# Optimization experiments

Measured on AMD Instinct MI355X. Metric: run time of the kernel, lower is better.

## Reference

```python
import jax, jax.numpy as jnp
import numpy as np

DIM = 1024
N_HEADS = 16
HEAD_DIM = DIM // N_HEADS
COND_DIM = 1024
MLP_RATIO = 4
B, S = 4, 1024
LN_EPS = 1e-5


def _layer_norm(x, w):
    # F.layer_norm without affine bias, then * weight (per original LayerNorm)
    x32 = x.astype(jnp.float32)
    mu = jnp.mean(x32, axis=-1, keepdims=True)
    var = jnp.var(x32, axis=-1, keepdims=True)
    return (x32 - mu) * jax.lax.rsqrt(var + LN_EPS) * w


def _rope(t, cos, sin):
    # t: [b, s, h, d]; cos/sin: [s, d/2]; rotate-half convention
    d2 = t.shape[-1] // 2
    t1, t2 = t[..., :d2], t[..., d2:]
    c = cos[None, :, None, :]
    s = sin[None, :, None, :]
    return jnp.concatenate([t1 * c - t2 * s, t2 * c + t1 * s], axis=-1)


def setup_inputs() -> dict:
    key = jax.random.key(0)
    ks = jax.random.split(key, 12)
    inv_freq = 1.0 / (10000.0 ** (np.arange(0, HEAD_DIM, 2) / HEAD_DIM))
    ang = np.arange(S)[:, None] * inv_freq[None, :]
    return {
        "x": jax.random.normal(ks[0], (B, S, DIM), jnp.float32),
        "cos": jnp.asarray(np.cos(ang), jnp.float32),
        "sin": jnp.asarray(np.sin(ang), jnp.float32),
        "c": jax.random.normal(ks[1], (B, COND_DIM), jnp.float32),
        "w_ln1": jnp.ones((DIM,), jnp.float32),
        "w_ln2": jnp.ones((DIM,), jnp.float32),
        "w_qkv": jax.random.normal(ks[2], (DIM, 3 * DIM), jnp.float32) * 0.02,
        "w_attn_out": jax.random.normal(ks[3], (DIM, DIM), jnp.float32) * 0.02,
        "w_mlp1": jax.random.normal(ks[4], (DIM, MLP_RATIO * DIM), jnp.float32) * 0.02,
        "b_mlp1": jnp.zeros((MLP_RATIO * DIM,), jnp.float32),
        "w_mlp2": jax.random.normal(ks[5], (MLP_RATIO * DIM, DIM), jnp.float32) * 0.02,
        "b_mlp2": jnp.zeros((DIM,), jnp.float32),
        "w_ada": jax.random.normal(ks[6], (COND_DIM, 6 * DIM), jnp.float32) * 0.02,
        "b_ada": jax.random.normal(ks[7], (6 * DIM,), jnp.float32) * 0.02,
    }


def reference(x, cos, sin, c, w_ln1, w_ln2, w_qkv, w_attn_out,
              w_mlp1, b_mlp1, w_mlp2, b_mlp2, w_ada, b_ada):
    b, s, dim = x.shape
    # adaLN modulation: [b, 6*dim] -> six [b, 1, dim] chunks
    mod = (c @ w_ada + b_ada)[:, None, :]
    shift_msa, scale_msa, gate_msa, shift_mlp, scale_mlp, gate_mlp = jnp.split(mod, 6, axis=2)

    x_skip = x
    h = _layer_norm(x, w_ln1) * (1.0 + scale_msa) + shift_msa
    qkv = (h @ w_qkv).reshape(b, s, 3, N_HEADS, HEAD_DIM)
    q = _rope(qkv[:, :, 0], cos, sin)
    k = _rope(qkv[:, :, 1], cos, sin)
    v = qkv[:, :, 2]

    scale = 1.0 / jnp.sqrt(jnp.asarray(HEAD_DIM, x.dtype))
    scores = jnp.einsum('bshd,bthd->bhst', q, k) * scale  # [b,h,s,s]
    attn = jax.nn.softmax(scores, axis=-1)
    o = jnp.einsum('bhst,bthd->bshd', attn, v).reshape(b, s, dim)

    x = x_skip + gate_msa * (o @ w_attn_out)

    h2 = _layer_norm(x, w_ln2) * (1.0 + scale_mlp) + shift_mlp
    m = jax.nn.gelu(h2 @ w_mlp1 + b_mlp1, approximate=True) @ w_mlp2 + b_mlp2
    return x + gate_mlp * m
```

## Files before the change

kernel.cpp:

```cpp
#include <hip/hip_runtime.h>
#include <stdint.h>

typedef unsigned short u16;
typedef __bf16 bf16x8 __attribute__((ext_vector_type(8)));
typedef float f32x4 __attribute__((ext_vector_type(4)));

#define MOD6  6144

__device__ __forceinline__ float b2f(unsigned int u) {
    union { unsigned int i; float f; } z; z.i = u << 16; return z.f;
}
__device__ __forceinline__ u16 f2b(float f) {
    union { float f; unsigned int i; } z; z.f = f;
    unsigned int i = z.i;
    return (u16)((i + 0x7fffu + ((i >> 16) & 1u)) >> 16);
}
union U4 { uint4 u; u16 s[8]; };
union U2 { uint2 u; u16 s[4]; };
union B8 { bf16x8 v; unsigned int w[4]; };

__device__ __forceinline__ float ldf(const void* p, size_t i, int isbf) {
    if (isbf) return b2f(((const u16*)p)[i]);
    return ((const float*)p)[i];
}
__device__ __forceinline__ void load4(const void* p, size_t i, int isbf, float* v) {
    if (isbf) {
        U2 t; t.u = *(const uint2*)((const u16*)p + i);
#pragma unroll
        for (int e = 0; e < 4; e++) v[e] = b2f(t.s[e]);
    } else {
        float4 f = *(const float4*)((const float*)p + i);
        v[0] = f.x; v[1] = f.y; v[2] = f.z; v[3] = f.w;
    }
}

__device__ __forceinline__ void gld16(u16* lds, const u16* g) {
    __builtin_amdgcn_global_load_lds(
        (__attribute__((address_space(1))) void*)(g),
        (__attribute__((address_space(3))) void*)(lds), 16, 0, 0);
}

__global__ void detect_dtype(const unsigned int* __restrict__ w, int* __restrict__ flag) {
    if (threadIdx.x == 0 && blockIdx.x == 0)
        *flag = (w[0] == 0x3F803F80u) ? 1 : 0;
}

__global__ void transpose_any(const void* __restrict__ in, u16* __restrict__ out,
                              int K, int N, const int* __restrict__ flag) {
    const int isbf = *flag;
    __shared__ u16 tile[64][66];
    const int ntn = N >> 6;
    const int k0 = (blockIdx.x / ntn) << 6;
    const int n0 = (blockIdx.x % ntn) << 6;
    const int tid = threadIdx.x;
    const int r = tid >> 3;
    const int c = (tid & 7) * 8;
#pragma unroll
    for (int rr = 0; rr < 64; rr += 32) {
        const size_t base = (size_t)(k0 + r + rr) * N + n0 + c;
        u16* t = &tile[r + rr][c];
        if (isbf) {
            U4 v; v.u = *(const uint4*)((const u16*)in + base);
#pragma unroll
            for (int e = 0; e < 8; e++) t[e] = v.s[e];
        } else {
            float4 a = *(const float4*)((const float*)in + base);
            float4 b = *(const float4*)((const float*)in + base + 4);
            t[0] = f2b(a.x); t[1] = f2b(a.y); t[2] = f2b(a.z); t[3] = f2b(a.w);
            t[4] = f2b(b.x); t[5] = f2b(b.y); t[6] = f2b(b.z); t[7] = f2b(b.w);
        }
    }
    __syncthreads();
#pragma unroll
    for (int rr = 0; rr < 64; rr += 32) {
        U4 v;
#pragma unroll
        for (int e = 0; e < 8; e++) v.s[e] = tile[c + e][r + rr];
        *(uint4*)&out[(size_t)(n0 + r + rr) * K + k0 + c] = v.u;
    }
}

__global__ void ada_partial(const void* __restrict__ c, const void* __restrict__ w_ada,
                            float* __restrict__ part, const int* __restrict__ flag) {
    const int isbf = *flag;
    const int g = blockIdx.x * 256 + threadIdx.x;
    const int slice = g / 24576;
    const int idx = g - slice * 24576;
    const int b = idx / MOD6, n = idx - (idx / MOD6) * MOD6;
    const int k0 = slice * 128;
    float acc = 0.f;
    if (isbf) {
        const u16* cr = (const u16*)c + b * 1024 + k0;
        const u16* wp = (const u16*)w_ada + (size_t)k0 * MOD6 + n;
#pragma unroll 8
        for (int k = 0; k < 128; k++)
            acc += b2f(cr[k]) * b2f(wp[(size_t)k * MOD6]);
    } else {
        const float* cr = (const float*)c + b * 1024 + k0;
        const float* wp = (const float*)w_ada + (size_t)k0 * MOD6 + n;
#pragma unroll 8
        for (int k = 0; k < 128; k++)
            acc += cr[k] * wp[(size_t)k * MOD6];
    }
    part[g] = acc;
}
__global__ void ada_reduce(const float* __restrict__ part, const void* __restrict__ b_ada,
                           float* __restrict__ mod, const int* __restrict__ flag) {
    const int g = blockIdx.x * 256 + threadIdx.x;
    float acc = ldf(b_ada, g % MOD6, *flag);
#pragma unroll
    for (int s = 0; s < 8; s++) acc += part[s * 24576 + g];
    mod[g] = acc;
}

__global__ void ln_mod_kernel(const void* __restrict__ x, const void* __restrict__ w,
                              const float* __restrict__ mod, int shift_off,
                              int scale_off, u16* __restrict__ out,
                              const int* __restrict__ flag, int x_is_f32) {
    const int isbf = *flag;
    const int xb = x_is_f32 ? 0 : isbf;
    const int tk = blockIdx.x;
    const int b = tk >> 10;
    const int tid = threadIdx.x;
    float v[4];
    load4(x, (size_t)tk * 1024 + tid * 4, xb, v);
    float s = v[0] + v[1] + v[2] + v[3];
    float ss = v[0]*v[0] + v[1]*v[1] + v[2]*v[2] + v[3]*v[3];
#pragma unroll
    for (int off = 1; off < 64; off <<= 1) {
        s  += __shfl_xor(s, off);
        ss += __shfl_xor(ss, off);
    }
    __shared__ float ls[4], lss[4];
    if ((tid & 63) == 0) { ls[tid >> 6] = s; lss[tid >> 6] = ss; }
    __syncthreads();
    s  = ls[0] + ls[1] + ls[2] + ls[3];
    ss = lss[0] + lss[1] + lss[2] + lss[3];
    const float mu  = s * (1.f / 1024.f);
    const float var = ss * (1.f / 1024.f) - mu * mu;
    const float rstd = rsqrtf(var + 1e-5f);
    float wv[4];
    load4(w, (size_t)tid * 4, isbf, wv);
    const float* mb = mod + (size_t)b * MOD6;
    U2 o;
#pragma unroll
    for (int e = 0; e < 4; e++) {
        const int col = tid * 4 + e;
        float n = (v[e] - mu) * rstd * wv[e];
        o.s[e] = f2b(n * (1.f + mb[scale_off + col]) + mb[shift_off + col]);
    }
    *(uint2*)(out + (size_t)tk * 1024 + tid * 4) = o.u;
}

__global__ void out_init(const float* __restrict__ res, const float* __restrict__ gate,
                         const void* __restrict__ bias, float* __restrict__ out,
                         const int* __restrict__ flag) {
    const int isbf = *flag;
    const int g = blockIdx.x * 256 + threadIdx.x;
    const int col = (g & 255) * 4;
    const int row = g >> 8;
    const int b = row >> 10;
    float bv[4];
    load4(bias, (size_t)col, isbf, bv);
    const float* gp = gate + (size_t)b * MOD6 + col;
    float4 r = *(const float4*)(res + (size_t)row * 1024 + col);
    float4 o;
    o.x = r.x + gp[0] * bv[0];
    o.y = r.y + gp[1] * bv[1];
    o.z = r.z + gp[2] * bv[2];
    o.w = r.w + gp[3] * bv[3];
    *(float4*)(out + (size_t)row * 1024 + col) = o;
}

#define EPI_STORE 0
#define EPI_RES_GATE 1
#define EPI_GELU_BIAS 2
#define EPI_RES_GATE_BIAS 3
#define EPI_ATOMIC_GATE 4

template <int EPI>
__launch_bounds__(256, 2)
__global__ void gemm_bt(const u16* __restrict__ A, const u16* __restrict__ Bt,
                        void* __restrict__ Cv, int M, int N, int K,
                        const void* __restrict__ res, const float* __restrict__ gate,
                        const void* __restrict__ bias, const int* __restrict__ flag,
                        int Ks) {
    __shared__ __align__(16) u16 sA[128 * 32];
    __shared__ __align__(16) u16 sB[128 * 32];
    const int isbf = flag ? *flag : 0;
    const int tid = threadIdx.x;
    const int lane = tid & 63;
    const int w = tid >> 6;
    const int wm = w >> 1, wn = w & 1;
    const int c16 = lane & 15, quad = lane >> 4;
    const int m0 = blockIdx.y * 128, n0 = blockIdx.x * 128;
    const int kt0 = blockIdx.z * Ks;

    const int srow = lane >> 2;
    const int schunk = lane & 3;
    const int gchunk = schunk ^ (srow & 3);

    const u16* gA = A + (size_t)m0 * K + 8 * gchunk;
    const u16* gB = Bt + (size_t)n0 * K + 8 * gchunk;
    const int cs = quad ^ (c16 & 3);

    f32x4 acc[4][4];
#pragma unroll
    for (int i = 0; i < 4; i++)
#pragma unroll
        for (int j = 0; j < 4; j++) acc[i][j] = (f32x4){0.f, 0.f, 0.f, 0.f};

#pragma unroll 1
    for (int kt = kt0; kt < kt0 + Ks; kt += 32) {
        __syncthreads();
#pragma unroll
        for (int p = 0; p < 2; p++) {
            const int r = 16 * (w + 4 * p) + srow;
            gld16(&sA[r * 32 + 8 * schunk], gA + (size_t)r * K + kt);
            gld16(&sB[r * 32 + 8 * schunk], gB + (size_t)r * K + kt);
        }
        __syncthreads();
        bf16x8 af[4], bfr[4];
#pragma unroll
        for (int i = 0; i < 4; i++)
            af[i] = *(const bf16x8*)&sA[(64 * wm + 16 * i + c16) * 32 + 8 * cs];
#pragma unroll
        for (int j = 0; j < 4; j++)
            bfr[j] = *(const bf16x8*)&sB[(64 * wn + 16 * j + c16) * 32 + 8 * cs];
#pragma unroll
        for (int i = 0; i < 4; i++)
#pragma unroll
            for (int j = 0; j < 4; j++)
                acc[i][j] = __builtin_amdgcn_mfma_f32_16x16x32_bf16(
                    af[i], bfr[j], acc[i][j], 0, 0, 0);
    }

#pragma unroll
    for (int i = 0; i < 4; i++) {
#pragma unroll
        for (int r = 0; r < 4; r++) {
            const int row = m0 + 64 * wm + 16 * i + 4 * quad + r;
            const int b = row >> 10;
#pragma unroll
            for (int j = 0; j < 4; j++) {
                const int col = n0 + 64 * wn + 16 * j + c16;
                float v = acc[i][j][r];
                if constexpr (EPI == EPI_GELU_BIAS) {
                    v += ldf(bias, col, isbf);
                    const float u = 0.7978845608f * (v + 0.044715f * v * v * v);
                    const float e = __expf(2.f * u);
                    const float t = 1.f - 2.f / (e + 1.f);
                    v = 0.5f * v * (1.f + t);
                } else if constexpr (EPI == EPI_RES_GATE) {
                    v = ldf(res, (size_t)row * N + col, isbf)
                        + gate[(size_t)b * MOD6 + col] * v;
                } else if constexpr (EPI == EPI_RES_GATE_BIAS) {
                    v += ldf(bias, col, isbf);
                    v = ((const float*)res)[(size_t)row * N + col]
                        + gate[(size_t)b * MOD6 + col] * v;
                }
                if constexpr (EPI == EPI_ATOMIC_GATE) {
                    atomicAdd((float*)Cv + (size_t)row * N + col,
                              gate[(size_t)b * MOD6 + col] * v);
                } else if constexpr (EPI == EPI_RES_GATE || EPI == EPI_RES_GATE_BIAS) {
                    ((float*)Cv)[(size_t)row * N + col] = v;
                } else {
                    ((u16*)Cv)[(size_t)row * N + col] = f2b(v);
                }
            }
        }
    }
}

__global__ void rope_kernel(u16* __restrict__ qkv, const void* __restrict__ cosb,
                            const void* __restrict__ sinb, const int* __restrict__ flag) {
    const int isbf = *flag;
    const int g = blockIdx.x * 256 + threadIdx.x;
    const int q8 = g & 7;
    const int h = (g >> 3) & 15;
    const int tk = g >> 7;
    const int s = tk & 1023;
    const int d = q8 * 4;
    u16* row = qkv + (size_t)tk * 3072;

    float c4[4], s4[4];
    load4(cosb, (size_t)s * 32 + d, isbf, c4);
    load4(sinb, (size_t)s * 32 + d, isbf, s4);

#pragma unroll
    for (int which = 0; which < 2; which++) {
        u16* p1 = row + which * 1024 + h * 64 + d;
        u16* p2 = p1 + 32;
        U2 t1, t2;
        t1.u = *(const uint2*)p1;
        t2.u = *(const uint2*)p2;
        U2 o1, o2;
#pragma unroll
        for (int e = 0; e < 4; e++) {
            const float a = b2f(t1.s[e]), bb = b2f(t2.s[e]);
            o1.s[e] = f2b(a * c4[e] - bb * s4[e]);
            o2.s[e] = f2b(bb * c4[e] + a * s4[e]);
        }
        *(uint2*)p1 = o1.u;
        *(uint2*)p2 = o2.u;
    }
}

__launch_bounds__(256, 4)
__global__ void attn_mfma(const u16* __restrict__ qkv, u16* __restrict__ o_out) {
    __shared__ __align__(16) u16 sK[64 * 72];
    __shared__ __align__(16) u16 sVt[64 * 72];
    const int bh = blockIdx.x >> 4;
    const int qt = blockIdx.x & 15;
    const int b = bh >> 4, h = bh & 15;
    const int tid = threadIdx.x;
    const int w = tid >> 6;
    const int lane = tid & 63;
    const int c = lane & 15;
    const int quad = lane >> 4;

    const int q0 = qt * 64 + w * 16;
    bf16x8 qf0, qf1;
    {
        const u16* qrow = qkv + (size_t)(b * 1024 + q0 + c) * 3072 + h * 64;
        qf0 = *(const bf16x8*)(qrow + quad * 8);
        qf1 = *(const bf16x8*)(qrow + 32 + quad * 8);
    }
    f32x4 of[4];
#pragma unroll
    for (int dt = 0; dt < 4; dt++) of[dt] = (f32x4){0.f, 0.f, 0.f, 0.f};
    float mI = -1e30f, lI = 0.f;

    const int skey = tid >> 3;
    const int sch  = tid & 7;
    const int src0 = (((2 * quad) & 3) << 4) + c;
    const int src1 = (((2 * quad + 1) & 3) << 4) + c;

#pragma unroll 1
    for (int kt = 0; kt < 1024; kt += 64) {
        __syncthreads();
#pragma unroll
        for (int p = 0; p < 2; p++) {
            const int key = skey + p * 32;
            const u16* krow = qkv + (size_t)(b * 1024 + kt + key) * 3072 + 1024
                              + h * 64 + sch * 8;
            uint4 kv = *(const uint4*)krow;
            *(uint4*)&sK[key * 72 + sch * 8] = kv;
            U4 vv; vv.u = *(const uint4*)(krow + 1024);
#pragma unroll
            for (int e = 0; e < 8; e++) sVt[(sch * 8 + e) * 72 + key] = vv.s[e];
        }
        __syncthreads();
#pragma unroll
        for (int ks = 0; ks < 64; ks += 32) {
            bf16x8 k00 = *(const bf16x8*)&sK[(ks + c) * 72 + quad * 8];
            bf16x8 k01 = *(const bf16x8*)&sK[(ks + c) * 72 + 32 + quad * 8];
            bf16x8 k10 = *(const bf16x8*)&sK[(ks + 16 + c) * 72 + quad * 8];
            bf16x8 k11 = *(const bf16x8*)&sK[(ks + 16 + c) * 72 + 32 + quad * 8];
            f32x4 s0 = (f32x4){0.f, 0.f, 0.f, 0.f};
            f32x4 s1 = (f32x4){0.f, 0.f, 0.f, 0.f};
            s0 = __builtin_amdgcn_mfma_f32_16x16x32_bf16(k00, qf0, s0, 0, 0, 0);
            s0 = __builtin_amdgcn_mfma_f32_16x16x32_bf16(k01, qf1, s0, 0, 0, 0);
            s1 = __builtin_amdgcn_mfma_f32_16x16x32_bf16(k10, qf0, s1, 0, 0, 0);
            s1 = __builtin_amdgcn_mfma_f32_16x16x32_bf16(k11, qf1, s1, 0, 0, 0);
            float sc[8];
#pragma unroll
            for (int r = 0; r < 4; r++) { sc[r] = s0[r] * 0.125f; sc[4 + r] = s1[r] * 0.125f; }
            float tm = sc[0];
#pragma unroll
            for (int j = 1; j < 8; j++) tm = fmaxf(tm, sc[j]);
            tm = fmaxf(tm, __shfl_xor(tm, 16));
            tm = fmaxf(tm, __shfl_xor(tm, 32));
            const float mNew = fmaxf(mI, tm);
            const float alpha = __expf(mI - mNew);
            float p8[8];
            float psum = 0.f;
#pragma unroll
            for (int j = 0; j < 8; j++) { p8[j] = __expf(sc[j] - mNew); psum += p8[j]; }
            psum += __shfl_xor(psum, 16);
            psum += __shfl_xor(psum, 32);
            lI = lI * alpha + psum;
            mI = mNew;
#pragma unroll
            for (int dt = 0; dt < 4; dt++) {
#pragma unroll
                for (int r = 0; r < 4; r++) of[dt][r] *= alpha;
            }
            const unsigned int a0 = (unsigned)f2b(p8[0]) | ((unsigned)f2b(p8[1]) << 16);
            const unsigned int a1 = (unsigned)f2b(p8[2]) | ((unsigned)f2b(p8[3]) << 16);
            const unsigned int b0 = (unsigned)f2b(p8[4]) | ((unsigned)f2b(p8[5]) << 16);
            const unsigned int b1 = (unsigned)f2b(p8[6]) | ((unsigned)f2b(p8[7]) << 16);
            const unsigned int xa0 = (unsigned)__shfl((int)a0, src0);
            const unsigned int xb0 = (unsigned)__shfl((int)b0, src0);
            const unsigned int xa1 = (unsigned)__shfl((int)a1, src0);
            const unsigned int xb1 = (unsigned)__shfl((int)b1, src0);
            const unsigned int ya0 = (unsigned)__shfl((int)a0, src1);
            const unsigned int yb0 = (unsigned)__shfl((int)b0, src1);
            const unsigned int ya1 = (unsigned)__shfl((int)a1, src1);
            const unsigned int yb1 = (unsigned)__shfl((int)b1, src1);
            B8 pf;
            pf.w[0] = quad < 2 ? xa0 : xb0;
            pf.w[1] = quad < 2 ? xa1 : xb1;
            pf.w[2] = quad < 2 ? ya0 : yb0;
            pf.w[3] = quad < 2 ? ya1 : yb1;
#pragma unroll
            for (int dt = 0; dt < 4; dt++) {
                bf16x8 vf = *(const bf16x8*)&sVt[(dt * 16 + c) * 72 + ks + quad * 8];
                of[dt] = __builtin_amdgcn_mfma_f32_16x16x32_bf16(vf, pf.v, of[dt], 0, 0, 0);
            }
        }
    }
    const float inv = 1.f / lI;
    const size_t orow = (size_t)(b * 1024 + q0 + c) * 1024 + h * 64;
#pragma unroll
    for (int dt = 0; dt < 4; dt++) {
        U2 pk;
#pragma unroll
        for (int r = 0; r < 4; r++) pk.s[r] = f2b(of[dt][r] * inv);
        *(uint2*)(o_out + orow + dt * 16 + quad * 4) = pk.u;
    }
}

extern "C" void kernel_launch(void* const* d_in, const int* in_sizes, int n_in,
                              void* d_out, int out_size, void* d_ws, size_t ws_size,
                              hipStream_t stream) {
    (void)in_sizes; (void)n_in; (void)out_size; (void)ws_size;
    const void* x      = d_in[0];
    const void* cosb   = d_in[1];
    const void* sinb   = d_in[2];
    const void* c      = d_in[3];
    const void* w_ln1  = d_in[4];
    const void* w_ln2  = d_in[5];
    const void* w_qkv  = d_in[6];
    const void* w_attn = d_in[7];
    const void* w_mlp1 = d_in[8];
    const void* b_mlp1 = d_in[9];
    const void* w_mlp2 = d_in[10];
    const void* b_mlp2 = d_in[11];
    const void* w_ada  = d_in[12];
    const void* b_ada  = d_in[13];
    char* ws = (char*)d_ws;

    u16*   wT_qkv  = (u16*)(ws + 0);
    u16*   wT_attn = (u16*)(ws + 6291456);
    u16*   wT_mlp1 = (u16*)(ws + 8388608);
    u16*   wT_mlp2 = (u16*)(ws + 16777216);
    float* mod     = (float*)(ws + 25165824);
    u16*   hbuf    = (u16*)(ws + 25264128);
    u16*   big     = (u16*)(ws + 33652736);
    float* x2      = (float*)(ws + 67207168);
    int*   flag    = (int*)(ws + 83984384);
    float* part    = (float*)big;

    detect_dtype<<<1, 64, 0, stream>>>((const unsigned int*)w_ln1, flag);
    transpose_any<<<dim3(16 * 48), 256, 0, stream>>>(w_qkv, wT_qkv, 1024, 3072, flag);
    transpose_any<<<dim3(16 * 16), 256, 0, stream>>>(w_attn, wT_attn, 1024, 1024, flag);
    transpose_any<<<dim3(16 * 64), 256, 0, stream>>>(w_mlp1, wT_mlp1, 1024, 4096, flag);
    transpose_any<<<dim3(64 * 16), 256, 0, stream>>>(w_mlp2, wT_mlp2, 4096, 1024, flag);
    ada_partial<<<768, 256, 0, stream>>>(c, w_ada, part, flag);
    ada_reduce<<<96, 256, 0, stream>>>(part, b_ada, mod, flag);
    ln_mod_kernel<<<4096, 256, 0, stream>>>(x, w_ln1, mod, 0, 1024, hbuf, flag, 0);
    gemm_bt<EPI_STORE><<<dim3(24, 32), 256, 0, stream>>>(
        hbuf, wT_qkv, big, 4096, 3072, 1024, nullptr, nullptr, nullptr, flag, 1024);
    rope_kernel<<<2048, 256, 0, stream>>>(big, cosb, sinb, flag);
    attn_mfma<<<1024, 256, 0, stream>>>(big, hbuf);
    gemm_bt<EPI_RES_GATE><<<dim3(8, 32), 256, 0, stream>>>(
        hbuf, wT_attn, x2, 4096, 1024, 1024, x, mod + 2048, nullptr, flag, 1024);
    ln_mod_kernel<<<4096, 256, 0, stream>>>(x2, w_ln2, mod, 3072, 4096, hbuf, flag, 1);
    out_init<<<4096, 256, 0, stream>>>(x2, mod + 5120, b_mlp2, (float*)d_out, flag);
    gemm_bt<EPI_GELU_BIAS><<<dim3(32, 32), 256, 0, stream>>>(
        hbuf, wT_mlp1, big, 4096, 4096, 1024, nullptr, nullptr, b_mlp1, flag, 1024);
    gemm_bt<EPI_ATOMIC_GATE><<<dim3(8, 32, 4), 256, 0, stream>>>(
        big, wT_mlp2, (float*)d_out, 4096, 1024, 4096, nullptr, mod + 5120, nullptr,
        flag, 1024);
}
```

Baseline: 474.3 us.

## Double-buffer GEMM shared tiles and remap blocks across XCDs for cache locality

The GEMM now uses two shared-memory buffers, prefetching the next K-tile with async global-to-LDS loads while MFMAs run on the current tile, so one barrier per iteration replaces two. Block indices in both the GEMM and the attention kernel are remapped so that blocks dispatched round-robin to the 8 XCDs get contiguous M/head ranges, which should improve L2 reuse. The cost is doubled LDS per block, which may limit occupancy, and the remap assumes grid dimensions divisible by 8.

Measured after the change: 460.6 us. 2.9% less time.

```diff
diff --git a/kernel.cpp b/kernel.cpp
--- a/kernel.cpp
+++ b/kernel.cpp
@@ -185,54 +185,85 @@
                         const void* __restrict__ res, const float* __restrict__ gate,
                         const void* __restrict__ bias, const int* __restrict__ flag,
                         int Ks) {
-    __shared__ __align__(16) u16 sA[128 * 32];
-    __shared__ __align__(16) u16 sB[128 * 32];
+    __shared__ __align__(16) u16 sA[2][128 * 32];
+    __shared__ __align__(16) u16 sB[2][128 * 32];
     const int isbf = flag ? *flag : 0;
     const int tid = threadIdx.x;
     const int lane = tid & 63;
     const int w = tid >> 6;
     const int wm = w >> 1, wn = w & 1;
     const int c16 = lane & 15, quad = lane >> 4;
-    const int m0 = blockIdx.y * 128, n0 = blockIdx.x * 128;
-    const int kt0 = blockIdx.z * Ks;
+
+    int bx, by, bz;
+    {
+        const int nx = gridDim.x, ny = gridDim.y, nz = gridDim.z;
+        const int flat = blockIdx.x + nx * (blockIdx.y + ny * blockIdx.z);
+        const int q = flat & 7;
+        const int s = flat >> 3;
+        const int g = s / nx;
+        bx = s - g * nx;
+        const int p = q * ((ny * nz) >> 3) + g;
+        by = p % ny;
+        bz = p / ny;
+    }
+    const int m0 = by * 128, n0 = bx * 128;
+    const int kt0 = bz * Ks;
 
     const int srow = lane >> 2;
     const int schunk = lane & 3;
     const int gchunk = schunk ^ (srow & 3);
 
-    const u16* gA = A + (size_t)m0 * K + 8 * gchunk;
-    const u16* gB = Bt + (size_t)n0 * K + 8 * gchunk;
+    const u16* gA = A + (size_t)m0 * K + 8 * gchunk + kt0;
+    const u16* gB = Bt + (size_t)n0 * K + 8 * gchunk + kt0;
     const int cs = quad ^ (c16 & 3);
 
+    const int r0 = 16 * w + srow;
+    const int r1 = r0 + 64;
+    const int d0 = r0 * 32 + 8 * schunk;
+    const int d1 = r1 * 32 + 8 * schunk;
+
     f32x4 acc[4][4];
 #pragma unroll
     for (int i = 0; i < 4; i++)
 #pragma unroll
         for (int j = 0; j < 4; j++) acc[i][j] = (f32x4){0.f, 0.f, 0.f, 0.f};
 
+    gld16(&sA[0][d0], gA + (size_t)r0 * K);
+    gld16(&sB[0][d0], gB + (size_t)r0 * K);
+    gld16(&sA[0][d1], gA + (size_t)r1 * K);
+    gld16(&sB[0][d1], gB + (size_t)r1 * K);
+    __syncthreads();
+
+    const int nt = Ks >> 5;
+    int cur = 0;
 #pragma unroll 1
-    for (int kt = kt0; kt < kt0 + Ks; kt += 32) {
-        __syncthreads();
-#pragma unroll
-        for (int p = 0; p < 2; p++) {
-            const int r = 16 * (w + 4 * p) + srow;
-            gld16(&sA[r * 32 + 8 * schunk], gA + (size_t)r * K + kt);
-            gld16(&sB[r * 32 + 8 * schunk], gB + (size_t)r * K + kt);
+    for (int t = 0; t < nt; ++t) {
+        if (t + 1 < nt) {
+            const int kt = (t + 1) << 5;
+            u16* dA = &sA[cur ^ 1][0];
+            u16* dB = &sB[cur ^ 1][0];
+            gld16(dA + d0, gA + (size_t)r0 * K + kt);
+            gld16(dB + d0, gB + (size_t)r0 * K + kt);
+            gld16(dA + d1, gA + (size_t)r1 * K + kt);
+            gld16(dB + d1, gB + (size_t)r1 * K + kt);
         }
-        __syncthreads();
+        const u16* fA = &sA[cur][0];
+        const u16* fB = &sB[cur][0];
         bf16x8 af[4], bfr[4];
 #pragma unroll
         for (int i = 0; i < 4; i++)
-            af[i] = *(const bf16x8*)&sA[(64 * wm + 16 * i + c16) * 32 + 8 * cs];
+            af[i] = *(const bf16x8*)&fA[(64 * wm + 16 * i + c16) * 32 + 8 * cs];
 #pragma unroll
         for (int j = 0; j < 4; j++)
-            bfr[j] = *(const bf16x8*)&sB[(64 * wn + 16 * j + c16) * 32 + 8 * cs];
+            bfr[j] = *(const bf16x8*)&fB[(64 * wn + 16 * j + c16) * 32 + 8 * cs];
 #pragma unroll
         for (int i = 0; i < 4; i++)
 #pragma unroll
             for (int j = 0; j < 4; j++)
                 acc[i][j] = __builtin_amdgcn_mfma_f32_16x16x32_bf16(
                     af[i], bfr[j], acc[i][j], 0, 0, 0);
+        __syncthreads();
+        cur ^= 1;
     }
 
 #pragma unroll
@@ -310,8 +341,10 @@
 __global__ void attn_mfma(const u16* __restrict__ qkv, u16* __restrict__ o_out) {
     __shared__ __align__(16) u16 sK[64 * 72];
     __shared__ __align__(16) u16 sVt[64 * 72];
-    const int bh = blockIdx.x >> 4;
-    const int qt = blockIdx.x & 15;
+    const int flat = blockIdx.x;
+    const int xq = flat & 7, xs = flat >> 3;
+    const int qt = xs & 15;
+    const int bh = xq * 8 + (xs >> 4);
     const int b = bh >> 4, h = bh & 15;
     const int tid = threadIdx.x;
     const int w = tid >> 6;
```
